# Optimization experiments

Hardware: AMD Instinct MI355X
Metric: run time of the kernel (lower is better)

## Reference

```python
import jax, jax.numpy as jnp
import numpy as np

B, D_IN, D_H, D_OUT = 8192, 512, 256, 128
TEMP = 0.07
EPS_BN = 1e-5


def _bn(x, g, b):
    # BatchNorm1d in training mode: biased batch statistics
    mu = jnp.mean(x, axis=0)
    var = jnp.var(x, axis=0)
    return (x - mu) * jax.lax.rsqrt(var + EPS_BN) * g + b


def _project(x, W1, b1, g1, beta1, W2, b2, g2, beta2, W3, b3):
    h = jax.nn.relu(_bn(x @ W1 + b1, g1, beta1))
    h = jax.nn.relu(_bn(h @ W2 + b2, g2, beta2))
    return h @ W3 + b3  # (B, D_OUT)


def setup_inputs() -> dict:
    key = jax.random.key(0)
    ks = jax.random.split(key, 6)
    f32 = jnp.float32
    return {
        "x1": jax.random.normal(ks[0], (B, D_IN), f32),
        "x2": jax.random.normal(ks[1], (B, D_IN), f32),
        "W1": jax.random.normal(ks[2], (D_IN, D_H), f32) * 0.04,
        "b1": jnp.zeros((D_H,), f32),
        "g1": jnp.ones((D_H,), f32),
        "beta1": jnp.zeros((D_H,), f32),
        "W2": jax.random.normal(ks[3], (D_H, D_H), f32) * 0.06,
        "b2": jnp.zeros((D_H,), f32),
        "g2": jnp.ones((D_H,), f32),
        "beta2": jnp.zeros((D_H,), f32),
        "W3": jax.random.normal(ks[4], (D_H, D_OUT), f32) * 0.06,
        "b3": jnp.zeros((D_OUT,), f32),
    }


def reference(x1, x2, W1, b1, g1, beta1, W2, b2, g2, beta2, W3, b3):
    z1 = _project(x1, W1, b1, g1, beta1, W2, b2, g2, beta2, W3, b3)
    z2 = _project(x2, W1, b1, g1, beta1, W2, b2, g2, beta2, W3, b3)
    # F.normalize(dim=1), eps=1e-12
    z1 = z1 / jnp.maximum(jnp.linalg.norm(z1, axis=1, keepdims=True), 1e-12)
    z2 = z2 / jnp.maximum(jnp.linalg.norm(z2, axis=1, keepdims=True), 1e-12)
    reps = jnp.concatenate([z1, z2], axis=0)           # (2B, D)
    # cosine similarity of unit vectors == single GEMM (2B, 2B)
    sim = reps @ reps.T
    idx = jnp.arange(B)
    positives = jnp.concatenate([sim[idx, idx + B], sim[idx + B, idx]], axis=0)  # (2B,)
    nominator = jnp.exp(positives / TEMP)
    # source bug preserved: denominator sums sim/temp (no exp), masking the diagonal
    denominator = (jnp.sum(sim, axis=1) - jnp.diagonal(sim)) / TEMP
    loss = -jnp.log(nominator / denominator)
    return jnp.mean(loss)
```

## Files before the change

kernel.cpp:

```cpp
#include <hip/hip_runtime.h>
#include <math.h>

#define BATCH   8192
#define MROWS   16384
#define DIN     512
#define DH      256
#define DOUT    128
#define EPS_BN  1e-5f
#define TEMP    0.07f

using f4    = __attribute__((ext_vector_type(4))) float;
using f32x4 = __attribute__((ext_vector_type(4))) float;
using h4    = __attribute__((ext_vector_type(4))) _Float16;
using h8    = __attribute__((ext_vector_type(8))) _Float16;

#define GLD_LDS16(gp, lp) __builtin_amdgcn_global_load_lds( \
    (const __attribute__((address_space(1))) void*)(gp),    \
    (__attribute__((address_space(3))) void*)(lp), 16, 0, 0)

#define VMCNT(n) asm volatile("s_waitcnt vmcnt(" #n ")" ::: "memory")
#define LGKM0()  asm volatile("s_waitcnt lgkmcnt(0)" ::: "memory")

template <int K, int N, int FUSE_BN, int EPI>
__global__ __launch_bounds__(256, 2) void gemm_fused(
    const float* __restrict__ A1, const float* __restrict__ A2, int splitRow,
    const _Float16* __restrict__ BThi, const _Float16* __restrict__ BTlo,
    const float* __restrict__ stats, const float* __restrict__ g,
    const float* __restrict__ beta, const float* __restrict__ bias,
    float* __restrict__ Cout, float* __restrict__ red)
{
    constexpr int NT = K / 32;

    const int tid = threadIdx.x;
    const int wave = tid >> 6, lane = tid & 63;
    const int wr = wave >> 1, wc = wave & 1;
    const int l4 = lane >> 4, lc = lane & 15;
    const int wg = blockIdx.x;
    const int brow = (wg & 255) * 64;
    const int bcol = (wg >> 8) * 128;
    const int half = (brow >= BATCH) ? 1 : 0;

    __shared__ __align__(16) char smem[75776];
    _Float16* Bring = (_Float16*)smem;
    _Float16* Aring = (_Float16*)(smem + 49152);
    float*    scsh  = (float*)(smem + 73728);
    float*    sR    = (float*)(smem + 49152);
    float*    nLp   = (float*)(smem + 49152 + 8192);

    const _Float16* bsrc[4];
    {
        const int co = (bcol + wave * 32 + lc) * K + l4 * 8;
        bsrc[0] = BThi + co;
        bsrc[1] = BThi + co + 16 * K;
        bsrc[2] = BTlo + co;
        bsrc[3] = BTlo + co + 16 * K;
    }
    auto stageB = [&](int buf, int t) {
        _Float16* d = Bring + buf * 8192 + wave * 1024;
        GLD_LDS16(bsrc[0] + t * 32, d);
        GLD_LDS16(bsrc[1] + t * 32, d + 512);
        GLD_LDS16(bsrc[2] + t * 32, d + 4096);
        GLD_LDS16(bsrc[3] + t * 32, d + 4096 + 512);
    };

    const int arow = wave * 16 + lc;
    const int ak0 = l4 * 8;
    const int growA = brow + arow;
    const float* asrc = (growA < splitRow)
        ? (A1 + (size_t)growA * K + ak0)
        : (A2 + (size_t)(growA - splitRow) * K + ak0);

    f4 ar[3][2];
    auto loadA = [&](int p, int t) {
        ar[p][0] = *(const f4*)(asrc + t * 32);
        ar[p][1] = *(const f4*)(asrc + t * 32 + 4);
    };
    auto procA = [&](int p, int buf, int t) {
        float v[8];
#pragma unroll
        for (int j = 0; j < 4; ++j) { v[j] = ar[p][0][j]; v[4 + j] = ar[p][1][j]; }
        if constexpr (FUSE_BN) {
            f4 s0 = *(const f4*)&scsh[t * 32 + ak0];
            f4 s1 = *(const f4*)&scsh[t * 32 + ak0 + 4];
            f4 h0 = *(const f4*)&scsh[256 + t * 32 + ak0];
            f4 h1 = *(const f4*)&scsh[256 + t * 32 + ak0 + 4];
#pragma unroll
            for (int j = 0; j < 4; ++j) {
                v[j]     = fmaxf(fmaf(v[j],     s0[j], h0[j]), 0.f);
                v[4 + j] = fmaxf(fmaf(v[4 + j], s1[j], h1[j]), 0.f);
            }
        }
        h8 hi, lo;
#pragma unroll
        for (int j = 0; j < 8; ++j) {
            _Float16 h = (_Float16)v[j];
            hi[j] = h;
            lo[j] = (_Float16)(v[j] - (float)h);
        }
        _Float16* d = Aring + buf * 4096 + wave * 512 + lane * 8;
        *(h8*)d = hi;
        *(h8*)(d + 2048) = lo;
    };

    f32x4 acc[2][4];
#pragma unroll
    for (int mi = 0; mi < 2; ++mi)
#pragma unroll
        for (int ni = 0; ni < 4; ++ni)
#pragma unroll
            for (int c = 0; c < 4; ++c) acc[mi][ni][c] = 0.f;

    auto compute = [&](int buf) {
        const _Float16* Ab = Aring + buf * 4096;
        const _Float16* Bb = Bring + buf * 8192;
        h8 ah[2], al[2], bh[4], bl[4];
#pragma unroll
        for (int mi = 0; mi < 2; ++mi) {
            ah[mi] = *(const h8*)(Ab + (wr * 2 + mi) * 512 + lane * 8);
            al[mi] = *(const h8*)(Ab + 2048 + (wr * 2 + mi) * 512 + lane * 8);
        }
#pragma unroll
        for (int ni = 0; ni < 4; ++ni) {
            bh[ni] = *(const h8*)(Bb + (wc * 4 + ni) * 512 + lane * 8);
            bl[ni] = *(const h8*)(Bb + 4096 + (wc * 4 + ni) * 512 + lane * 8);
        }
        __builtin_amdgcn_s_setprio(1);
#pragma unroll
        for (int mi = 0; mi < 2; ++mi)
#pragma unroll
            for (int ni = 0; ni < 4; ++ni) {
                acc[mi][ni] = __builtin_amdgcn_mfma_f32_16x16x32_f16(
                    ah[mi], bh[ni], acc[mi][ni], 0, 0, 0);
                acc[mi][ni] = __builtin_amdgcn_mfma_f32_16x16x32_f16(
                    al[mi], bh[ni], acc[mi][ni], 0, 0, 0);
                acc[mi][ni] = __builtin_amdgcn_mfma_f32_16x16x32_f16(
                    ah[mi], bl[ni], acc[mi][ni], 0, 0, 0);
            }
        __builtin_amdgcn_s_setprio(0);
    };

    float st0, st1, gv, bt;
    if constexpr (FUSE_BN) {
        st0 = stats[half * 512 + tid];
        st1 = stats[half * 512 + 256 + tid];
        gv = g[tid];
        bt = beta[tid];
    }
    loadA(0, 0);
    loadA(1, 1);
    loadA(2, 2);
    stageB(0, 0);
    stageB(1, 1);
    if constexpr (FUSE_BN) {
        const float invN = 1.0f / (float)BATCH;
        float mu = st0 * invN;
        float var = fmaf(-mu, mu, st1 * invN);
        float s = gv * rsqrtf(var + EPS_BN);
        scsh[tid] = s;
        scsh[256 + tid] = fmaf(-mu, s, bt);
        LGKM0();
        __builtin_amdgcn_s_barrier();
    }
    procA(0, 0, 0);
    loadA(0, 3);
    VMCNT(6);
    LGKM0();
    __builtin_amdgcn_s_barrier();

#pragma unroll
    for (int t = 0; t < NT; ++t) {
        if (t + 2 < NT) stageB((t + 2) % 3, t + 2);
        compute(t % 3);
        if (t + 1 < NT) {
            if (t + 3 < NT)      VMCNT(6);
            else if (t + 2 < NT) VMCNT(4);
            else                 VMCNT(0);
            __builtin_amdgcn_sched_barrier(0);
            procA((t + 1) % 3, (t + 1) % 3, t + 1);
            if (t + 4 < NT) loadA((t + 4) % 3, t + 4);
        }
        LGKM0();
        __builtin_amdgcn_s_barrier();
    }
    __syncthreads();

    float bv[4];
#pragma unroll
    for (int ni = 0; ni < 4; ++ni) bv[ni] = bias[bcol + wc * 64 + ni * 16 + lc];

    if constexpr (EPI == 0) {
        float s[4] = {}, q[4] = {};
#pragma unroll
        for (int mi = 0; mi < 2; ++mi)
#pragma unroll
            for (int j = 0; j < 4; ++j) {
                int gr = brow + wr * 32 + mi * 16 + l4 * 4 + j;
#pragma unroll
                for (int ni = 0; ni < 4; ++ni) {
                    float v = acc[mi][ni][j] + bv[ni];
                    Cout[(size_t)gr * N + bcol + wc * 64 + ni * 16 + lc] = v;
                    s[ni] += v;
                    q[ni] = fmaf(v, v, q[ni]);
                }
            }
#pragma unroll
        for (int ni = 0; ni < 4; ++ni) {
            sR[(wr * 4 + l4) * 128 + wc * 64 + ni * 16 + lc] = s[ni];
            sR[1024 + (wr * 4 + l4) * 128 + wc * 64 + ni * 16 + lc] = q[ni];
        }
        __syncthreads();
        if (tid < 128) {
            float ss = 0.f, qq = 0.f;
#pragma unroll
            for (int i = 0; i < 8; ++i) {
                ss += sR[i * 128 + tid];
                qq += sR[1024 + i * 128 + tid];
            }
            atomicAdd(&red[half * 512 + bcol + tid], ss);
            atomicAdd(&red[half * 512 + 256 + bcol + tid], qq);
        }
    } else {
        float v[2][4][4];
#pragma unroll
        for (int mi = 0; mi < 2; ++mi)
#pragma unroll
            for (int j = 0; j < 4; ++j) {
                float ssq = 0.f;
#pragma unroll
                for (int ni = 0; ni < 4; ++ni) {
                    v[mi][j][ni] = acc[mi][ni][j] + bv[ni];
                    ssq = fmaf(v[mi][j][ni], v[mi][j][ni], ssq);
                }
#pragma unroll
                for (int o = 1; o < 16; o <<= 1) ssq += __shfl_xor(ssq, o);
                if (lc == 0) nLp[(wr * 32 + mi * 16 + l4 * 4 + j) * 2 + wc] = ssq;
            }
        __syncthreads();
        float s[4] = {};
#pragma unroll
        for (int mi = 0; mi < 2; ++mi)
#pragma unroll
            for (int j = 0; j < 4; ++j) {
                int lrow = wr * 32 + mi * 16 + l4 * 4 + j;
                float tot = nLp[lrow * 2] + nLp[lrow * 2 + 1];
                float inv = 1.0f / fmaxf(sqrtf(tot), 1e-12f);
#pragma unroll
                for (int ni = 0; ni < 4; ++ni) {
                    float z = v[mi][j][ni] * inv;
                    Cout[(size_t)(brow + lrow) * DOUT + wc * 64 + ni * 16 + lc] = z;
                    s[ni] += z;
                }
            }
        __syncthreads();
#pragma unroll
        for (int ni = 0; ni < 4; ++ni)
            sR[(wr * 4 + l4) * 128 + wc * 64 + ni * 16 + lc] = s[ni];
        __syncthreads();
        if (tid < 128) {
            float ss = 0.f;
#pragma unroll
            for (int i = 0; i < 8; ++i) ss += sR[i * 128 + tid];
            atomicAdd(&red[tid], ss);
        }
    }
}

__global__ __launch_bounds__(256) void wprep(
    const float* __restrict__ W1, const float* __restrict__ W2,
    const float* __restrict__ W3,
    _Float16* __restrict__ W1hiT, _Float16* __restrict__ W1loT,
    _Float16* __restrict__ W2hiT, _Float16* __restrict__ W2loT,
    _Float16* __restrict__ W3hiT, _Float16* __restrict__ W3loT,
    float* __restrict__ smalls, float* __restrict__ out)
{
    const int b = blockIdx.x;
    if (b == 56) {
        for (int i = threadIdx.x; i < 2176; i += 256) smalls[i] = 0.f;
        if (threadIdx.x == 0) out[0] = 0.f;
        return;
    }
#pragma unroll
    for (int i = 0; i < 4; ++i) {
        int qd = b * 1024 + i * 256 + threadIdx.x;
        const float* src; _Float16 *dhi, *dlo; int n, kq, Nw, Kw;
        if (qd < 32768)      { src = W1; dhi = W1hiT; dlo = W1loT;
                               n = qd & 255;            kq = qd >> 8; Nw = 256; Kw = 512; }
        else if (qd < 49152) { src = W2; dhi = W2hiT; dlo = W2loT;
                               n = (qd - 32768) & 255;  kq = (qd - 32768) >> 8; Nw = 256; Kw = 256; }
        else                 { src = W3; dhi = W3hiT; dlo = W3loT;
                               n = (qd - 49152) & 127;  kq = (qd - 49152) >> 7; Nw = 128; Kw = 256; }
        h4 hi, lo;
#pragma unroll
        for (int j = 0; j < 4; ++j) {
            float w = src[(size_t)(kq * 4 + j) * Nw + n];
            _Float16 h = (_Float16)w;
            hi[j] = h;
            lo[j] = (_Float16)(w - (float)h);
        }
        *(h4*)&dhi[(size_t)n * Kw + kq * 4] = hi;
        *(h4*)&dlo[(size_t)n * Kw + kq * 4] = lo;
    }
}

__global__ __launch_bounds__(256) void losspos(const float* __restrict__ reps,
                                               const float* __restrict__ Svec,
                                               float* __restrict__ out)
{
    const int lane = threadIdx.x & 63;
    const int grp = threadIdx.x >> 6;
    __shared__ float part[4];
    float2 sv = ((const float2*)Svec)[lane];
    float acc = 0.f;
#pragma unroll 1
    for (int it = 0; it < 4; ++it) {
        int p = blockIdx.x * 16 + it * 4 + grp;
        float2 a = ((const float2*)(reps + (size_t)p * DOUT))[lane];
        float2 b = ((const float2*)(reps + (size_t)(p + BATCH) * DOUT))[lane];
        float dp  = fmaf(a.x, b.x, a.y * b.y);
        float rsA = fmaf(a.x, sv.x, a.y * sv.y);
        float sdA = fmaf(a.x, a.x, a.y * a.y);
        float rsB = fmaf(b.x, sv.x, b.y * sv.y);
        float sdB = fmaf(b.x, b.x, b.y * b.y);
#pragma unroll
        for (int o = 32; o; o >>= 1) {
            dp  += __shfl_xor(dp, o);
            rsA += __shfl_xor(rsA, o);
            sdA += __shfl_xor(sdA, o);
            rsB += __shfl_xor(rsB, o);
            sdB += __shfl_xor(sdB, o);
        }
        if (lane == 0) {
            float nom = expf(dp / TEMP);
            float dA = (rsA - sdA) / TEMP;
            float dB = (rsB - sdB) / TEMP;
            acc += -logf(nom / dA) - logf(nom / dB);
        }
    }
    if (lane == 0) part[grp] = acc;
    __syncthreads();
    if (threadIdx.x == 0) {
        float t = part[0] + part[1] + part[2] + part[3];
        atomicAdd(out, t * (1.0f / (float)MROWS));
    }
}

extern "C" void kernel_launch(void* const* d_in, const int* in_sizes, int n_in,
                              void* d_out, int out_size, void* d_ws, size_t ws_size,
                              hipStream_t stream)
{
    const float* x1    = (const float*)d_in[0];
    const float* x2    = (const float*)d_in[1];
    const float* W1    = (const float*)d_in[2];
    const float* b1    = (const float*)d_in[3];
    const float* g1    = (const float*)d_in[4];
    const float* beta1 = (const float*)d_in[5];
    const float* W2    = (const float*)d_in[6];
    const float* b2    = (const float*)d_in[7];
    const float* g2    = (const float*)d_in[8];
    const float* beta2 = (const float*)d_in[9];
    const float* W3    = (const float*)d_in[10];
    const float* b3    = (const float*)d_in[11];
    float* out = (float*)d_out;

    char* W = (char*)d_ws;
    float*    Y1   = (float*)(W);
    float*    Y2   = (float*)(W + (16u << 20));
    float*    REPS = (float*)(W + (32u << 20));
    char* wb = W + (40u << 20);
    _Float16* W1HIT = (_Float16*)(wb);
    _Float16* W1LOT = (_Float16*)(wb + 262144);
    _Float16* W2HIT = (_Float16*)(wb + 524288);
    _Float16* W2LOT = (_Float16*)(wb + 655360);
    _Float16* W3HIT = (_Float16*)(wb + 786432);
    _Float16* W3LOT = (_Float16*)(wb + 851968);
    float* smalls   = (float*)  (wb + 917504);
    float* stats1 = smalls;
    float* stats2 = smalls + 1024;
    float* Svec   = smalls + 2048;

    const int big = 1 << 30;

    wprep<<<57, 256, 0, stream>>>(W1, W2, W3, W1HIT, W1LOT, W2HIT, W2LOT,
                                  W3HIT, W3LOT, smalls, out);

    gemm_fused<DIN, DH, 0, 0><<<512, 256, 0, stream>>>(
        x1, x2, BATCH, W1HIT, W1LOT, nullptr, nullptr, nullptr, b1, Y1, stats1);

    gemm_fused<DH, DH, 1, 0><<<512, 256, 0, stream>>>(
        Y1, Y1, big, W2HIT, W2LOT, stats1, g1, beta1, b2, Y2, stats2);

    gemm_fused<DH, DOUT, 1, 1><<<256, 256, 0, stream>>>(
        Y2, Y2, big, W3HIT, W3LOT, stats2, g2, beta2, b3, REPS, Svec);

    losspos<<<512, 256, 0, stream>>>(REPS, Svec, out);
}
```

Before: 169.0 us.

## Keep A fragments in registers, give each wave full tile width, transpose weights via LDS

The GEMM now has each wave own 16 rows across all 128 columns. Each lane's split-fp16 A fragment is kept in registers and fed straight to the MFMAs, instead of being staged through an LDS ring. This removes the A-tile LDS writes and reads, cuts shared memory so three workgroups can fit per CU, and lets the normalize epilogue reduce row norms inside one wave with no cross-wave LDS exchange. The weight-prep kernel now transposes 64x64 tiles through shared memory to get coalesced reads and writes. In exchange each wave holds more accumulators and reads every B fragment, which raises LDS B traffic per wave and register pressure under the tighter launch bound.

Measured after the change: 166.1 us. Within noise of the previous version (-1.7%).

```diff
diff --git a/kernel.cpp b/kernel.cpp
--- a/kernel.cpp
+++ b/kernel.cpp
@@ -22,7 +22,7 @@
 #define LGKM0()  asm volatile("s_waitcnt lgkmcnt(0)" ::: "memory")
 
 template <int K, int N, int FUSE_BN, int EPI>
-__global__ __launch_bounds__(256, 2) void gemm_fused(
+__global__ __launch_bounds__(256, 3) void gemm_fused(
     const float* __restrict__ A1, const float* __restrict__ A2, int splitRow,
     const _Float16* __restrict__ BThi, const _Float16* __restrict__ BTlo,
     const float* __restrict__ stats, const float* __restrict__ g,
@@ -33,19 +33,16 @@
 
     const int tid = threadIdx.x;
     const int wave = tid >> 6, lane = tid & 63;
-    const int wr = wave >> 1, wc = wave & 1;
     const int l4 = lane >> 4, lc = lane & 15;
     const int wg = blockIdx.x;
     const int brow = (wg & 255) * 64;
     const int bcol = (wg >> 8) * 128;
     const int half = (brow >= BATCH) ? 1 : 0;
 
-    __shared__ __align__(16) char smem[75776];
+    __shared__ __align__(16) char smem[51200];
     _Float16* Bring = (_Float16*)smem;
-    _Float16* Aring = (_Float16*)(smem + 49152);
-    float*    scsh  = (float*)(smem + 73728);
-    float*    sR    = (float*)(smem + 49152);
-    float*    nLp   = (float*)(smem + 49152 + 8192);
+    float*    scsh  = (float*)(smem + 49152);
+    float*    sR    = (float*)smem;
 
     const _Float16* bsrc[4];
     {
@@ -63,9 +60,8 @@
         GLD_LDS16(bsrc[3] + t * 32, d + 4096 + 512);
     };
 
-    const int arow = wave * 16 + lc;
+    const int growA = brow + wave * 16 + lc;
     const int ak0 = l4 * 8;
-    const int growA = brow + arow;
     const float* asrc = (growA < splitRow)
         ? (A1 + (size_t)growA * K + ak0)
         : (A2 + (size_t)(growA - splitRow) * K + ak0);
@@ -75,7 +71,8 @@
         ar[p][0] = *(const f4*)(asrc + t * 32);
         ar[p][1] = *(const f4*)(asrc + t * 32 + 4);
     };
-    auto procA = [&](int p, int buf, int t) {
+    h8 ah, al;
+    auto procA = [&](int p, int t) {
         float v[8];
 #pragma unroll
         for (int j = 0; j < 4; ++j) { v[j] = ar[p][0][j]; v[4 + j] = ar[p][1][j]; }
@@ -90,53 +87,42 @@
                 v[4 + j] = fmaxf(fmaf(v[4 + j], s1[j], h1[j]), 0.f);
             }
         }
-        h8 hi, lo;
 #pragma unroll
         for (int j = 0; j < 8; ++j) {
             _Float16 h = (_Float16)v[j];
-            hi[j] = h;
-            lo[j] = (_Float16)(v[j] - (float)h);
-        }
-        _Float16* d = Aring + buf * 4096 + wave * 512 + lane * 8;
-        *(h8*)d = hi;
-        *(h8*)(d + 2048) = lo;
+            ah[j] = h;
+            al[j] = (_Float16)(v[j] - (float)h);
+        }
     };
 
-    f32x4 acc[2][4];
-#pragma unroll
-    for (int mi = 0; mi < 2; ++mi)
-#pragma unroll
-        for (int ni = 0; ni < 4; ++ni)
-#pragma unroll
-            for (int c = 0; c < 4; ++c) acc[mi][ni][c] = 0.f;
+    f32x4 acc[8];
+#pragma unroll
+    for (int ni = 0; ni < 8; ++ni)
+#pragma unroll
+        for (int c = 0; c < 4; ++c) acc[ni][c] = 0.f;
 
     auto compute = [&](int buf) {
-        const _Float16* Ab = Aring + buf * 4096;
         const _Float16* Bb = Bring + buf * 8192;
-        h8 ah[2], al[2], bh[4], bl[4];
-#pragma unroll
-        for (int mi = 0; mi < 2; ++mi) {
-            ah[mi] = *(const h8*)(Ab + (wr * 2 + mi) * 512 + lane * 8);
-            al[mi] = *(const h8*)(Ab + 2048 + (wr * 2 + mi) * 512 + lane * 8);
-        }
-#pragma unroll
-        for (int ni = 0; ni < 4; ++ni) {
-            bh[ni] = *(const h8*)(Bb + (wc * 4 + ni) * 512 + lane * 8);
-            bl[ni] = *(const h8*)(Bb + 4096 + (wc * 4 + ni) * 512 + lane * 8);
-        }
-        __builtin_amdgcn_s_setprio(1);
-#pragma unroll
-        for (int mi = 0; mi < 2; ++mi)
+#pragma unroll
+        for (int hf = 0; hf < 2; ++hf) {
+            h8 bh[4], bl[4];
 #pragma unroll
             for (int ni = 0; ni < 4; ++ni) {
-                acc[mi][ni] = __builtin_amdgcn_mfma_f32_16x16x32_f16(
-                    ah[mi], bh[ni], acc[mi][ni], 0, 0, 0);
-                acc[mi][ni] = __builtin_amdgcn_mfma_f32_16x16x32_f16(
-                    al[mi], bh[ni], acc[mi][ni], 0, 0, 0);
-                acc[mi][ni] = __builtin_amdgcn_mfma_f32_16x16x32_f16(
-                    ah[mi], bl[ni], acc[mi][ni], 0, 0, 0);
-            }
-        __builtin_amdgcn_s_setprio(0);
+                bh[ni] = *(const h8*)(Bb + (hf * 4 + ni) * 512 + lane * 8);
+                bl[ni] = *(const h8*)(Bb + 4096 + (hf * 4 + ni) * 512 + lane * 8);
+            }
+            __builtin_amdgcn_s_setprio(1);
+#pragma unroll
+            for (int ni = 0; ni < 4; ++ni) {
+                acc[hf * 4 + ni] = __builtin_amdgcn_mfma_f32_16x16x32_f16(
+                    ah, bh[ni], acc[hf * 4 + ni], 0, 0, 0);
+                acc[hf * 4 + ni] = __builtin_amdgcn_mfma_f32_16x16x32_f16(
+                    al, bh[ni], acc[hf * 4 + ni], 0, 0, 0);
+                acc[hf * 4 + ni] = __builtin_amdgcn_mfma_f32_16x16x32_f16(
+                    ah, bl[ni], acc[hf * 4 + ni], 0, 0, 0);
+            }
+            __builtin_amdgcn_s_setprio(0);
+        }
     };
 
     float st0, st1, gv, bt;
@@ -146,11 +132,11 @@
         gv = g[tid];
         bt = beta[tid];
     }
+    stageB(0, 0);
     loadA(0, 0);
+    stageB(1, 1);
     loadA(1, 1);
     loadA(2, 2);
-    stageB(0, 0);
-    stageB(1, 1);
     if constexpr (FUSE_BN) {
         const float invN = 1.0f / (float)BATCH;
         float mu = st0 * invN;
@@ -161,10 +147,8 @@
         LGKM0();
         __builtin_amdgcn_s_barrier();
     }
-    procA(0, 0, 0);
-    loadA(0, 3);
-    VMCNT(6);
-    LGKM0();
+    procA(0, 0);
+    VMCNT(8);
     __builtin_amdgcn_s_barrier();
 
 #pragma unroll
@@ -172,94 +156,80 @@
         if (t + 2 < NT) stageB((t + 2) % 3, t + 2);
         compute(t % 3);
         if (t + 1 < NT) {
-            if (t + 3 < NT)      VMCNT(6);
-            else if (t + 2 < NT) VMCNT(4);
+            if (t + 3 < NT) loadA((t + 3) % 3, t + 3);
+            if (t + 3 < NT)      VMCNT(8);
+            else if (t + 2 < NT) VMCNT(6);
             else                 VMCNT(0);
             __builtin_amdgcn_sched_barrier(0);
-            procA((t + 1) % 3, (t + 1) % 3, t + 1);
-            if (t + 4 < NT) loadA((t + 4) % 3, t + 4);
-        }
-        LGKM0();
-        __builtin_amdgcn_s_barrier();
+            procA((t + 1) % 3, t + 1);
+            __builtin_amdgcn_s_barrier();
+        }
     }
     __syncthreads();
 
-    float bv[4];
-#pragma unroll
-    for (int ni = 0; ni < 4; ++ni) bv[ni] = bias[bcol + wc * 64 + ni * 16 + lc];
+    float bv[8];
+#pragma unroll
+    for (int ni = 0; ni < 8; ++ni) bv[ni] = bias[bcol + ni * 16 + lc];
 
     if constexpr (EPI == 0) {
-        float s[4] = {}, q[4] = {};
-#pragma unroll
-        for (int mi = 0; mi < 2; ++mi)
-#pragma unroll
-            for (int j = 0; j < 4; ++j) {
-                int gr = brow + wr * 32 + mi * 16 + l4 * 4 + j;
-#pragma unroll
-                for (int ni = 0; ni < 4; ++ni) {
-                    float v = acc[mi][ni][j] + bv[ni];
-                    Cout[(size_t)gr * N + bcol + wc * 64 + ni * 16 + lc] = v;
-                    s[ni] += v;
-                    q[ni] = fmaf(v, v, q[ni]);
-                }
-            }
-#pragma unroll
-        for (int ni = 0; ni < 4; ++ni) {
-            sR[(wr * 4 + l4) * 128 + wc * 64 + ni * 16 + lc] = s[ni];
-            sR[1024 + (wr * 4 + l4) * 128 + wc * 64 + ni * 16 + lc] = q[ni];
+        float s[8] = {}, q[8] = {};
+#pragma unroll
+        for (int j = 0; j < 4; ++j) {
+            int gr = brow + wave * 16 + l4 * 4 + j;
+#pragma unroll
+            for (int ni = 0; ni < 8; ++ni) {
+                float v = acc[ni][j] + bv[ni];
+                Cout[(size_t)gr * N + bcol + ni * 16 + lc] = v;
+                s[ni] += v;
+                q[ni] = fmaf(v, v, q[ni]);
+            }
+        }
+#pragma unroll
+        for (int ni = 0; ni < 8; ++ni) {
+            sR[(wave * 4 + l4) * 128 + ni * 16 + lc] = s[ni];
+            sR[2048 + (wave * 4 + l4) * 128 + ni * 16 + lc] = q[ni];
         }
         __syncthreads();
         if (tid < 128) {
             float ss = 0.f, qq = 0.f;
 #pragma unroll
-            for (int i = 0; i < 8; ++i) {
+            for (int i = 0; i < 16; ++i) {
                 ss += sR[i * 128 + tid];
-                qq += sR[1024 + i * 128 + tid];
+                qq += sR[2048 + i * 128 + tid];
             }
             atomicAdd(&red[half * 512 + bcol + tid], ss);
             atomicAdd(&red[half * 512 + 256 + bcol + tid], qq);
         }
     } else {
-        float v[2][4][4];
-#pragma unroll
-        for (int mi = 0; mi < 2; ++mi)
-#pragma unroll
-            for (int j = 0; j < 4; ++j) {
-                float ssq = 0.f;
-#pragma unroll
-                for (int ni = 0; ni < 4; ++ni) {
-                    v[mi][j][ni] = acc[mi][ni][j] + bv[ni];
-                    ssq = fmaf(v[mi][j][ni], v[mi][j][ni], ssq);
-                }
-#pragma unroll
-                for (int o = 1; o < 16; o <<= 1) ssq += __shfl_xor(ssq, o);
-                if (lc == 0) nLp[(wr * 32 + mi * 16 + l4 * 4 + j) * 2 + wc] = ssq;
-            }
-        __syncthreads();
-        float s[4] = {};
-#pragma unroll
-        for (int mi = 0; mi < 2; ++mi)
-#pragma unroll
-            for (int j = 0; j < 4; ++j) {
-                int lrow = wr * 32 + mi * 16 + l4 * 4 + j;
-                float tot = nLp[lrow * 2] + nLp[lrow * 2 + 1];
-                float inv = 1.0f / fmaxf(sqrtf(tot), 1e-12f);
-#pragma unroll
-                for (int ni = 0; ni < 4; ++ni) {
-                    float z = v[mi][j][ni] * inv;
-                    Cout[(size_t)(brow + lrow) * DOUT + wc * 64 + ni * 16 + lc] = z;
-                    s[ni] += z;
-                }
-            }
-        __syncthreads();
-#pragma unroll
-        for (int ni = 0; ni < 4; ++ni)
-            sR[(wr * 4 + l4) * 128 + wc * 64 + ni * 16 + lc] = s[ni];
+        float s[8] = {};
+#pragma unroll
+        for (int j = 0; j < 4; ++j) {
+            float vj[8];
+            float ssq = 0.f;
+#pragma unroll
+            for (int ni = 0; ni < 8; ++ni) {
+                vj[ni] = acc[ni][j] + bv[ni];
+                ssq = fmaf(vj[ni], vj[ni], ssq);
+            }
+#pragma unroll
+            for (int o = 1; o < 16; o <<= 1) ssq += __shfl_xor(ssq, o);
+            float inv = 1.0f / fmaxf(sqrtf(ssq), 1e-12f);
+            int gr = brow + wave * 16 + l4 * 4 + j;
+#pragma unroll
+            for (int ni = 0; ni < 8; ++ni) {
+                float z = vj[ni] * inv;
+                Cout[(size_t)gr * DOUT + ni * 16 + lc] = z;
+                s[ni] += z;
+            }
+        }
+#pragma unroll
+        for (int ni = 0; ni < 8; ++ni)
+            sR[(wave * 4 + l4) * 128 + ni * 16 + lc] = s[ni];
         __syncthreads();
         if (tid < 128) {
             float ss = 0.f;
 #pragma unroll
-            for (int i = 0; i < 8; ++i) ss += sR[i * 128 + tid];
+            for (int i = 0; i < 16; ++i) ss += sR[i * 128 + tid];
             atomicAdd(&red[tid], ss);
         }
     }
@@ -279,26 +249,38 @@
         if (threadIdx.x == 0) out[0] = 0.f;
         return;
     }
-#pragma unroll
-    for (int i = 0; i < 4; ++i) {
-        int qd = b * 1024 + i * 256 + threadIdx.x;
-        const float* src; _Float16 *dhi, *dlo; int n, kq, Nw, Kw;
-        if (qd < 32768)      { src = W1; dhi = W1hiT; dlo = W1loT;
-                               n = qd & 255;            kq = qd >> 8; Nw = 256; Kw = 512; }
-        else if (qd < 49152) { src = W2; dhi = W2hiT; dlo = W2loT;
-                               n = (qd - 32768) & 255;  kq = (qd - 32768) >> 8; Nw = 256; Kw = 256; }
-        else                 { src = W3; dhi = W3hiT; dlo = W3loT;
-                               n = (qd - 49152) & 127;  kq = (qd - 49152) >> 7; Nw = 128; Kw = 256; }
+    const float* src; _Float16 *dhi, *dlo; int Nw, Kw, kb, nb;
+    if (b < 32)      { src = W1; dhi = W1hiT; dlo = W1loT; Nw = 256; Kw = 512;
+                       kb = b >> 2; nb = b & 3; }
+    else if (b < 48) { int r = b - 32; src = W2; dhi = W2hiT; dlo = W2loT;
+                       Nw = 256; Kw = 256; kb = r >> 2; nb = r & 3; }
+    else             { int r = b - 48; src = W3; dhi = W3hiT; dlo = W3loT;
+                       Nw = 128; Kw = 256; kb = r >> 1; nb = r & 1; }
+
+    __shared__ float tile[64][65];
+    const int tx = threadIdx.x & 15, ty = threadIdx.x >> 4;
+#pragma unroll
+    for (int it = 0; it < 4; ++it) {
+        int kk = it * 16 + ty;
+        f4 v = *(const f4*)&src[(size_t)(kb * 64 + kk) * Nw + nb * 64 + tx * 4];
+#pragma unroll
+        for (int j = 0; j < 4; ++j) tile[kk][tx * 4 + j] = v[j];
+    }
+    __syncthreads();
+#pragma unroll
+    for (int it = 0; it < 4; ++it) {
+        int n = it * 16 + ty;
         h4 hi, lo;
 #pragma unroll
         for (int j = 0; j < 4; ++j) {
-            float w = src[(size_t)(kq * 4 + j) * Nw + n];
+            float w = tile[tx * 4 + j][n];
             _Float16 h = (_Float16)w;
             hi[j] = h;
             lo[j] = (_Float16)(w - (float)h);
         }
-        *(h4*)&dhi[(size_t)n * Kw + kq * 4] = hi;
-        *(h4*)&dlo[(size_t)n * Kw + kq * 4] = lo;
+        size_t o = (size_t)(nb * 64 + n) * Kw + kb * 64 + tx * 4;
+        *(h4*)&dhi[o] = hi;
+        *(h4*)&dlo[o] = lo;
     }
 }
 
```
